# Performance work log

Measured on AMD Instinct MI355X. Metric: run time of the kernel, lower is better.

The kernel has to match this reference:

```python
import jax, jax.numpy as jnp
import numpy as np

N_USERS = 100_000
N_ITEMS = 50_000
N_NODES = N_USERS + N_ITEMS
D = 64
NUM_LAYERS = 3
N_INTER = 1_000_000  # interactions; symmetrized -> 2M directed edges
BATCH = 4096


def setup_inputs() -> dict:
    key = jax.random.key(0)
    k_u, k_i, k_r, k_c, k_uid, k_iid = jax.random.split(key, 6)
    user_embedding = jax.random.normal(k_u, (N_USERS, D), dtype=jnp.float32)
    item_embedding = jax.random.normal(k_i, (N_ITEMS, D), dtype=jnp.float32)

    # build symmetric normalized adjacency edges as in get_norm_adj_mat
    rng = np.random.default_rng(0)
    row = rng.integers(0, N_USERS, size=N_INTER)
    col = rng.integers(0, N_ITEMS, size=N_INTER) + N_USERS
    src = np.concatenate([row, col])
    dst = np.concatenate([col, row])
    deg = np.bincount(src, minlength=N_NODES).astype(np.float32)
    norm_deg = 1.0 / np.sqrt(np.where(deg == 0, 1.0, deg))
    edge_weight = (norm_deg[src] * norm_deg[dst]).astype(np.float32)
    edge_index = np.stack([src, dst]).astype(np.int64)

    user_id = jax.random.randint(k_uid, (BATCH,), 0, N_USERS)
    item_id = jax.random.randint(k_iid, (BATCH,), 0, N_ITEMS)
    return {
        "user_embedding": user_embedding,
        "item_embedding": item_embedding,
        "edge_weight": jnp.asarray(edge_weight),
        "edge_index": jnp.asarray(edge_index),
        "user_id": user_id,
        "item_id": item_id,
    }


def reference(user_embedding, item_embedding, edge_weight, edge_index, user_id, item_id):
    # ego embeddings: [N_NODES, D]
    x = jnp.concatenate([user_embedding, item_embedding], axis=0)
    src, dst = edge_index[0], edge_index[1]
    h = x
    acc = x  # running sum over layer outputs (incl. layer 0)
    for _ in range(NUM_LAYERS):
        # LightGCNConv: gather source, scale by edge weight, scatter-add to dest
        msg = h[src] * edge_weight[:, None]                       # [E, D]
        h = jax.ops.segment_sum(msg, dst, num_segments=N_NODES)   # [N, D]
        acc = acc + h
    final = acc / jnp.asarray(NUM_LAYERS + 1, dtype=x.dtype)      # mean over layers
    u_embed = final[:N_USERS][user_id]
    i_embed = final[N_USERS:][item_id]
    return (u_embed, i_embed)
```

## Files before the change

kernel.cpp:

```cpp
#include <hip/hip_runtime.h>

#define N_USERS 100000
#define N_NODES 150000
#define DIM 64
#define BATCH 4096
#define BSHIFT 8
#define BUCKET 256
#define NB 586
#define NBP 768
#define PAIRS_PER_BLK 2048
#define STRIP 4096
#define CAPSHIFT 13
#define CAP (1 << CAPSHIFT)

typedef unsigned short bf16_t;

static __device__ __forceinline__ float bf2f(bf16_t h) {
    return __uint_as_float(((unsigned)h) << 16);
}
static __device__ __forceinline__ bf16_t f2bf(float f) {
    unsigned u = __float_as_uint(f);
    return (bf16_t)((u + 0x7FFFu + ((u >> 16) & 1u)) >> 16);
}

__global__ void __launch_bounds__(256)
lgcn_bin(const int* __restrict__ row, const int* __restrict__ col,
         int* __restrict__ pos, int* __restrict__ binned, int EH) {
    __shared__ int cnt[NBP];
    __shared__ int sA[256], sB[256];
    __shared__ int base[NB + 2];
    __shared__ int stage[STRIP];
    int tid = threadIdx.x;
    int k = blockIdx.x;
    cnt[tid] = 0; cnt[tid + 256] = 0; cnt[tid + 512] = 0;
    __syncthreads();
    int e0 = k * PAIRS_PER_BLK;
    int e1 = min(EH, e0 + PAIRS_PER_BLK);
    int n = e1 - e0;
    int nq = n >> 2;
    const int4* r4 = (const int4*)(row + e0);
    const int4* c4 = (const int4*)(col + e0);
    for (int q = tid; q < nq; q += 256) {
        int4 r = r4[q]; int4 c = c4[q];
        atomicAdd(&cnt[r.x >> BSHIFT], 1); atomicAdd(&cnt[c.x >> BSHIFT], 1);
        atomicAdd(&cnt[r.y >> BSHIFT], 1); atomicAdd(&cnt[c.y >> BSHIFT], 1);
        atomicAdd(&cnt[r.z >> BSHIFT], 1); atomicAdd(&cnt[c.z >> BSHIFT], 1);
        atomicAdd(&cnt[r.w >> BSHIFT], 1); atomicAdd(&cnt[c.w >> BSHIFT], 1);
    }
    __syncthreads();
    int c0 = cnt[3 * tid], c1 = cnt[3 * tid + 1], c2 = cnt[3 * tid + 2];
    int s = c0 + c1 + c2;
    sA[tid] = s;
    __syncthreads();
    int* c_ = sA; int* n_ = sB;
    for (int off = 1; off < 256; off <<= 1) {
        n_[tid] = (tid >= off) ? c_[tid] + c_[tid - off] : c_[tid];
        __syncthreads();
        int* t = c_; c_ = n_; n_ = t;
    }
    int excl = c_[tid] - s;
    if (3 * tid     <= NB) base[3 * tid]     = excl;
    if (3 * tid + 1 <= NB) base[3 * tid + 1] = excl + c0;
    if (3 * tid + 2 <= NB) base[3 * tid + 2] = excl + c0 + c1;
    __syncthreads();
    for (int i = tid; i <= NB; i += 256) {
        pos[k * (NB + 1) + i] = base[i];
        cnt[i] = base[i];
    }
    __syncthreads();
    for (int q = tid; q < nq; q += 256) {
        int4 r = r4[q]; int4 c = c4[q];
        int rr[4] = { r.x, r.y, r.z, r.w };
        int cc[4] = { c.x, c.y, c.z, c.w };
#pragma unroll
        for (int j = 0; j < 4; ++j) {
            int p1 = atomicAdd(&cnt[cc[j] >> BSHIFT], 1);
            stage[p1] = ((cc[j] & (BUCKET - 1)) << 18) | rr[j];
            int p2 = atomicAdd(&cnt[rr[j] >> BSHIFT], 1);
            stage[p2] = ((rr[j] & (BUCKET - 1)) << 18) | cc[j];
        }
    }
    __syncthreads();
    int m4 = (2 * n) >> 2;
    int4* dst = (int4*)(binned + k * STRIP);
    const int4* st4 = (const int4*)stage;
    for (int j = tid; j < m4; j += 256) dst[j] = st4[j];
}

__global__ void __launch_bounds__(256)
lgcn_build_csr(const int* __restrict__ pos, const int* __restrict__ binned,
               int4* __restrict__ nodeinfo, int* __restrict__ packed,
               const float* __restrict__ ue, const float* __restrict__ ie,
               bf16_t* __restrict__ g0, bf16_t* __restrict__ g1, int nblk) {
    __shared__ int stage[CAP];
    __shared__ int sorted[CAP];
    __shared__ int sA[256], sB[256];
    __shared__ int hist[256], cur[256];
    int b = blockIdx.x;
    int tid = threadIdx.x;
    int a0 = 0, l0 = 0, a1 = 0, l1 = 0;
    if (tid < nblk) {
        const int* pk = pos + tid * (NB + 1) + b;
        a0 = pk[0]; l0 = pk[1] - a0;
    }
    if (tid + 256 < nblk) {
        const int* pk = pos + (tid + 256) * (NB + 1) + b;
        a1 = pk[0]; l1 = pk[1] - a1;
    }
    int u = l0 + l1;
    sA[tid] = u;
    __syncthreads();
    int* c_ = sA; int* n_ = sB;
    for (int off = 1; off < 256; off <<= 1) {
        n_[tid] = (tid >= off) ? c_[tid] + c_[tid - off] : c_[tid];
        __syncthreads();
        int* t = c_; c_ = n_; n_ = t;
    }
    int myBase = c_[tid] - u;
    int Eb = c_[255];
    __syncthreads();
    {
        const int* s0 = binned + tid * STRIP + a0;
        int i = 0;
        for (; i + 4 <= l0; i += 4) {
            int w0 = s0[i], w1 = s0[i + 1], w2 = s0[i + 2], w3 = s0[i + 3];
            stage[myBase + i] = w0;     stage[myBase + i + 1] = w1;
            stage[myBase + i + 2] = w2; stage[myBase + i + 3] = w3;
        }
        for (; i < l0; ++i) stage[myBase + i] = s0[i];
        const int* s1 = binned + (tid + 256) * STRIP + a1;
        int bb = myBase + l0;
        i = 0;
        for (; i + 4 <= l1; i += 4) {
            int w0 = s1[i], w1 = s1[i + 1], w2 = s1[i + 2], w3 = s1[i + 3];
            stage[bb + i] = w0;     stage[bb + i + 1] = w1;
            stage[bb + i + 2] = w2; stage[bb + i + 3] = w3;
        }
        for (; i < l1; ++i) stage[bb + i] = s1[i];
    }
    hist[tid] = 0;
    __syncthreads();
    for (int j = tid; j < Eb; j += 256)
        atomicAdd(&hist[stage[j] >> 18], 1);
    __syncthreads();
    int deg = hist[tid];
    int degp = (deg + 3) & ~3;
    sA[tid] = degp;
    __syncthreads();
    int* c2 = sA; int* n2 = sB;
    for (int off = 1; off < 256; off <<= 1) {
        n2[tid] = (tid >= off) ? c2[tid] + c2[tid - off] : c2[tid];
        __syncthreads();
        int* t = c2; c2 = n2; n2 = t;
    }
    int startLoc = c2[tid] - degp;
    int totPad = c2[255];
    cur[tid] = startLoc;
    int gstart = (b << CAPSHIFT) + startLoc;
    int node = (b << BSHIFT) + tid;
    float da = (deg == 0) ? 1.0f : (float)deg;
    float sq = sqrtf(da);
    float nm = 1.0f / sq;
    if (node < N_NODES) {
        int4 ni;
        ni.x = gstart;
        ni.y = deg;
        ni.z = __float_as_int(nm);
        ni.w = __float_as_int(sq);
        nodeinfo[node] = ni;
    }
    __syncthreads();
    hist[tid] = __float_as_int(nm);
    for (int j = tid; j < totPad; j += 256) sorted[j] = N_NODES;
    __syncthreads();
    for (int j = tid; j < Eb; j += 256) {
        int w = stage[j];
        int p = atomicAdd(&cur[w >> 18], 1);
        sorted[p] = w & 0x3FFFF;
    }
    __syncthreads();
    int4* dst = (int4*)(packed + (b << CAPSHIFT));
    const int4* s4 = (const int4*)sorted;
    for (int j = tid; j < (totPad >> 2); j += 256) dst[j] = s4[j];
    int firstNode = b << BSHIFT;
    int nloc = min(BUCKET, N_NODES - firstNode);
    const int nU16 = N_USERS * (DIM / 4);
    int t0 = firstNode * (DIM / 4);
    for (int i = tid; i < nloc * (DIM / 4); i += 256) {
        int t = t0 + i;
        float4 x = (t < nU16) ? ((const float4*)ue)[t]
                              : ((const float4*)ie)[t - nU16];
        float nrm = __int_as_float(hist[i >> 4]);
        ushort4 o;
        o.x = f2bf(x.x * nrm); o.y = f2bf(x.y * nrm);
        o.z = f2bf(x.z * nrm); o.w = f2bf(x.w * nrm);
        ((ushort4*)g0)[t] = o;
    }
    if (b == 0 && tid < 32) {
        const int nT = N_NODES * (DIM / 4);
        if (tid < 16) ((ushort4*)g0)[nT + tid] = make_ushort4(0, 0, 0, 0);
        else          ((ushort4*)g1)[nT + tid - 16] = make_ushort4(0, 0, 0, 0);
    }
}


static __device__ __forceinline__ float4
gather_sum(const bf16_t* __restrict__ g, const int* __restrict__ packed,
           int start, int deg, int grp, int c) {
    float4 acc = make_float4(0.f, 0.f, 0.f, 0.f);
    for (int o = 4 * grp; o < deg; o += 16) {
        int4 e4 = *(const int4*)(packed + start + o);
        ushort4 v0 = ((const ushort4*)(g + (size_t)e4.x * DIM))[c];
        ushort4 v1 = ((const ushort4*)(g + (size_t)e4.y * DIM))[c];
        ushort4 v2 = ((const ushort4*)(g + (size_t)e4.z * DIM))[c];
        ushort4 v3 = ((const ushort4*)(g + (size_t)e4.w * DIM))[c];
        acc.x += bf2f(v0.x); acc.y += bf2f(v0.y);
        acc.z += bf2f(v0.z); acc.w += bf2f(v0.w);
        acc.x += bf2f(v1.x); acc.y += bf2f(v1.y);
        acc.z += bf2f(v1.z); acc.w += bf2f(v1.w);
        acc.x += bf2f(v2.x); acc.y += bf2f(v2.y);
        acc.z += bf2f(v2.z); acc.w += bf2f(v2.w);
        acc.x += bf2f(v3.x); acc.y += bf2f(v3.y);
        acc.z += bf2f(v3.z); acc.w += bf2f(v3.w);
    }
    return acc;
}

__global__ void __launch_bounds__(256)
lgcn_pull(const bf16_t* __restrict__ g, const int4* __restrict__ nodeinfo,
          const int* __restrict__ packed, bf16_t* __restrict__ gn) {
    int n = blockIdx.x * 4 + (threadIdx.x >> 6);
    if (n >= N_NODES) return;
    int lane = threadIdx.x & 63;
    int grp = lane >> 4;
    int c = lane & 15;
    int4 ni = nodeinfo[n];
    float4 acc = gather_sum(g, packed, ni.x, ni.y, grp, c);
#pragma unroll
    for (int off = 16; off < 64; off <<= 1) {
        acc.x += __shfl_xor(acc.x, off, 64);
        acc.y += __shfl_xor(acc.y, off, 64);
        acc.z += __shfl_xor(acc.z, off, 64);
        acc.w += __shfl_xor(acc.w, off, 64);
    }
    if (lane < 16) {
        float nm = __int_as_float(ni.z);
        float s2 = nm * nm;
        ushort4 o;
        o.x = f2bf(acc.x * s2); o.y = f2bf(acc.y * s2);
        o.z = f2bf(acc.z * s2); o.w = f2bf(acc.w * s2);
        ((ushort4*)(gn + (size_t)n * DIM))[c] = o;
    }
}

__global__ void __launch_bounds__(256)
lgcn_final(const float* __restrict__ ue, const float* __restrict__ ie,
           const bf16_t* __restrict__ g1, const bf16_t* __restrict__ g2,
           const int4* __restrict__ nodeinfo, const int* __restrict__ packed,
           const int* __restrict__ uid, const int* __restrict__ iid,
           float* __restrict__ out) {
    int slot = blockIdx.x * 4 + (threadIdx.x >> 6);
    if (slot >= 2 * BATCH) return;
    int lane = threadIdx.x & 63;
    int grp = lane >> 4;
    int c = lane & 15;
    int isItem = slot >= BATCH;
    int b = isItem ? (slot - BATCH) : slot;
    int node = isItem ? (N_USERS + iid[b]) : uid[b];
    int4 ni = nodeinfo[node];
    float4 acc = gather_sum(g2, packed, ni.x, ni.y, grp, c);
#pragma unroll
    for (int off = 16; off < 64; off <<= 1) {
        acc.x += __shfl_xor(acc.x, off, 64);
        acc.y += __shfl_xor(acc.y, off, 64);
        acc.z += __shfl_xor(acc.z, off, 64);
        acc.w += __shfl_xor(acc.w, off, 64);
    }
    if (lane < 16) {
        const float* xb = isItem ? (ie + (size_t)(node - N_USERS) * DIM)
                                 : (ue + (size_t)node * DIM);
        float4 x = ((const float4*)xb)[c];
        ushort4 a1 = ((const ushort4*)(g1 + (size_t)node * DIM))[c];
        ushort4 a2 = ((const ushort4*)(g2 + (size_t)node * DIM))[c];
        float rn = __int_as_float(ni.w);
        float nm = __int_as_float(ni.z);
        float4 r;
        r.x = 0.25f * (x.x + rn * (bf2f(a1.x) + bf2f(a2.x)) + nm * acc.x);
        r.y = 0.25f * (x.y + rn * (bf2f(a1.y) + bf2f(a2.y)) + nm * acc.y);
        r.z = 0.25f * (x.z + rn * (bf2f(a1.z) + bf2f(a2.z)) + nm * acc.z);
        r.w = 0.25f * (x.w + rn * (bf2f(a1.w) + bf2f(a2.w)) + nm * acc.w);
        ((float4*)(out + (size_t)slot * DIM))[c] = r;
    }
}


extern "C" void kernel_launch(void* const* d_in, const int* in_sizes, int n_in,
                              void* d_out, int out_size, void* d_ws, size_t ws_size,
                              hipStream_t stream) {
    const float* ue  = (const float*)d_in[0];
    const float* ie  = (const float*)d_in[1];
    const int*   ei  = (const int*)d_in[3];
    const int*   uid = (const int*)d_in[4];
    const int*   iid = (const int*)d_in[5];
    float* out = (float*)d_out;

    const int E  = in_sizes[2];
    const int EH = E / 2;
    const int* row = ei;
    const int* col = ei + E;

    const int nblk = (EH + PAIRS_PER_BLK - 1) / PAIRS_PER_BLK;

    char* p = (char*)d_ws;
    size_t off = 0;
    auto carve = [&](size_t bytes) -> char* {
        char* r = p + off;
        off += (bytes + 255) & ~(size_t)255;
        return r;
    };
    const size_t nodeBf16 = (size_t)(N_NODES + 1) * DIM * sizeof(bf16_t);
    bf16_t* gA       = (bf16_t*)carve(nodeBf16);
    bf16_t* gB       = (bf16_t*)carve(nodeBf16);
    int4*   nodeinfo = (int4*)carve((size_t)N_NODES * sizeof(int4));
    int*    pos      = (int*)carve((size_t)nblk * (NB + 1) * sizeof(int));
    int*    binned   = (int*)carve((size_t)nblk * STRIP * sizeof(int));
    int*    packed   = (int*)carve((size_t)NB * CAP * sizeof(int));
    (void)ws_size;

    lgcn_bin<<<nblk, 256, 0, stream>>>(row, col, pos, binned, EH);
    lgcn_build_csr<<<NB, 256, 0, stream>>>(pos, binned, nodeinfo, packed,
                                           ue, ie, gA, gB, nblk);
    const int pullGrid = (N_NODES + 3) / 4;
    lgcn_pull<<<pullGrid, 256, 0, stream>>>(gA, nodeinfo, packed, gB);
    lgcn_pull<<<pullGrid, 256, 0, stream>>>(gB, nodeinfo, packed, gA);
    lgcn_final<<<(2 * BATCH + 3) / 4, 256, 0, stream>>>(
        ue, ie, gB, gA, nodeinfo, packed, uid, iid, out);
}
```

Before: 229.8 us.

## Map one feature per lane in pull gather, drop cross-lane reduction

The neighbor gather changes from four 16-lane groups, each handling a quarter of the edges with 8-byte loads followed by a shuffle reduction, to all 64 lanes reading the same edge row one bf16 element per lane. The edge loop is unrolled by eight with scalar (readfirstlane) indices so the addresses stay uniform. This removes the shuffle reductions and the idle lanes in the epilogue, but each load is now 2 bytes per lane instead of 8 and each wave processes edges sequentially, so the number of memory instructions per edge goes up. Padded degree handling assumes the packed lists are padded to multiples of four with zero-row sentinels.

```diff
diff --git a/kernel.cpp b/kernel.cpp
--- a/kernel.cpp
+++ b/kernel.cpp
@@ -204,24 +204,38 @@
 }
 
 
-static __device__ __forceinline__ float4
-gather_sum(const bf16_t* __restrict__ g, const int* __restrict__ packed,
-           int start, int deg, int grp, int c) {
-    float4 acc = make_float4(0.f, 0.f, 0.f, 0.f);
-    for (int o = 4 * grp; o < deg; o += 16) {
-        int4 e4 = *(const int4*)(packed + start + o);
-        ushort4 v0 = ((const ushort4*)(g + (size_t)e4.x * DIM))[c];
-        ushort4 v1 = ((const ushort4*)(g + (size_t)e4.y * DIM))[c];
-        ushort4 v2 = ((const ushort4*)(g + (size_t)e4.z * DIM))[c];
-        ushort4 v3 = ((const ushort4*)(g + (size_t)e4.w * DIM))[c];
-        acc.x += bf2f(v0.x); acc.y += bf2f(v0.y);
-        acc.z += bf2f(v0.z); acc.w += bf2f(v0.w);
-        acc.x += bf2f(v1.x); acc.y += bf2f(v1.y);
-        acc.z += bf2f(v1.z); acc.w += bf2f(v1.w);
-        acc.x += bf2f(v2.x); acc.y += bf2f(v2.y);
-        acc.z += bf2f(v2.z); acc.w += bf2f(v2.w);
-        acc.x += bf2f(v3.x); acc.y += bf2f(v3.y);
-        acc.z += bf2f(v3.z); acc.w += bf2f(v3.w);
+static __device__ __forceinline__ float
+gather_lane(const bf16_t* __restrict__ g, const int* __restrict__ packed,
+            int su, int dp, int lane) {
+    float acc = 0.f;
+    const int4* p4 = (const int4*)(packed + su);
+    int k = 0;
+    for (; k + 8 <= dp; k += 8) {
+        int4 ea = p4[k >> 2];
+        int4 eb = p4[(k >> 2) + 1];
+        const bf16_t* r0 = g + ((unsigned)ea.x << 6);
+        const bf16_t* r1 = g + ((unsigned)ea.y << 6);
+        const bf16_t* r2 = g + ((unsigned)ea.z << 6);
+        const bf16_t* r3 = g + ((unsigned)ea.w << 6);
+        const bf16_t* r4 = g + ((unsigned)eb.x << 6);
+        const bf16_t* r5 = g + ((unsigned)eb.y << 6);
+        const bf16_t* r6 = g + ((unsigned)eb.z << 6);
+        const bf16_t* r7 = g + ((unsigned)eb.w << 6);
+        float v0 = bf2f(r0[lane]); float v1 = bf2f(r1[lane]);
+        float v2 = bf2f(r2[lane]); float v3 = bf2f(r3[lane]);
+        float v4 = bf2f(r4[lane]); float v5 = bf2f(r5[lane]);
+        float v6 = bf2f(r6[lane]); float v7 = bf2f(r7[lane]);
+        acc += ((v0 + v1) + (v2 + v3)) + ((v4 + v5) + (v6 + v7));
+    }
+    if (k < dp) {
+        int4 ea = p4[k >> 2];
+        const bf16_t* r0 = g + ((unsigned)ea.x << 6);
+        const bf16_t* r1 = g + ((unsigned)ea.y << 6);
+        const bf16_t* r2 = g + ((unsigned)ea.z << 6);
+        const bf16_t* r3 = g + ((unsigned)ea.w << 6);
+        float v0 = bf2f(r0[lane]); float v1 = bf2f(r1[lane]);
+        float v2 = bf2f(r2[lane]); float v3 = bf2f(r3[lane]);
+        acc += (v0 + v1) + (v2 + v3);
     }
     return acc;
 }
@@ -231,26 +245,15 @@
           const int* __restrict__ packed, bf16_t* __restrict__ gn) {
     int n = blockIdx.x * 4 + (threadIdx.x >> 6);
     if (n >= N_NODES) return;
+    n = __builtin_amdgcn_readfirstlane(n);
     int lane = threadIdx.x & 63;
-    int grp = lane >> 4;
-    int c = lane & 15;
     int4 ni = nodeinfo[n];
-    float4 acc = gather_sum(g, packed, ni.x, ni.y, grp, c);
-#pragma unroll
-    for (int off = 16; off < 64; off <<= 1) {
-        acc.x += __shfl_xor(acc.x, off, 64);
-        acc.y += __shfl_xor(acc.y, off, 64);
-        acc.z += __shfl_xor(acc.z, off, 64);
-        acc.w += __shfl_xor(acc.w, off, 64);
-    }
-    if (lane < 16) {
-        float nm = __int_as_float(ni.z);
-        float s2 = nm * nm;
-        ushort4 o;
-        o.x = f2bf(acc.x * s2); o.y = f2bf(acc.y * s2);
-        o.z = f2bf(acc.z * s2); o.w = f2bf(acc.w * s2);
-        ((ushort4*)(gn + (size_t)n * DIM))[c] = o;
-    }
+    int su = __builtin_amdgcn_readfirstlane(ni.x);
+    int du = __builtin_amdgcn_readfirstlane(ni.y);
+    int dp = (du + 3) & ~3;
+    float acc = gather_lane(g, packed, su, dp, lane);
+    float nm = __int_as_float(ni.z);
+    gn[((unsigned)n << 6) + lane] = f2bf(acc * nm * nm);
 }
 
 __global__ void __launch_bounds__(256)
@@ -261,36 +264,25 @@
            float* __restrict__ out) {
     int slot = blockIdx.x * 4 + (threadIdx.x >> 6);
     if (slot >= 2 * BATCH) return;
+    slot = __builtin_amdgcn_readfirstlane(slot);
     int lane = threadIdx.x & 63;
-    int grp = lane >> 4;
-    int c = lane & 15;
     int isItem = slot >= BATCH;
     int b = isItem ? (slot - BATCH) : slot;
     int node = isItem ? (N_USERS + iid[b]) : uid[b];
+    node = __builtin_amdgcn_readfirstlane(node);
     int4 ni = nodeinfo[node];
-    float4 acc = gather_sum(g2, packed, ni.x, ni.y, grp, c);
-#pragma unroll
-    for (int off = 16; off < 64; off <<= 1) {
-        acc.x += __shfl_xor(acc.x, off, 64);
-        acc.y += __shfl_xor(acc.y, off, 64);
-        acc.z += __shfl_xor(acc.z, off, 64);
-        acc.w += __shfl_xor(acc.w, off, 64);
-    }
-    if (lane < 16) {
-        const float* xb = isItem ? (ie + (size_t)(node - N_USERS) * DIM)
-                                 : (ue + (size_t)node * DIM);
-        float4 x = ((const float4*)xb)[c];
-        ushort4 a1 = ((const ushort4*)(g1 + (size_t)node * DIM))[c];
-        ushort4 a2 = ((const ushort4*)(g2 + (size_t)node * DIM))[c];
-        float rn = __int_as_float(ni.w);
-        float nm = __int_as_float(ni.z);
-        float4 r;
-        r.x = 0.25f * (x.x + rn * (bf2f(a1.x) + bf2f(a2.x)) + nm * acc.x);
-        r.y = 0.25f * (x.y + rn * (bf2f(a1.y) + bf2f(a2.y)) + nm * acc.y);
-        r.z = 0.25f * (x.z + rn * (bf2f(a1.z) + bf2f(a2.z)) + nm * acc.z);
-        r.w = 0.25f * (x.w + rn * (bf2f(a1.w) + bf2f(a2.w)) + nm * acc.w);
-        ((float4*)(out + (size_t)slot * DIM))[c] = r;
-    }
+    int su = __builtin_amdgcn_readfirstlane(ni.x);
+    int du = __builtin_amdgcn_readfirstlane(ni.y);
+    int dp = (du + 3) & ~3;
+    float acc = gather_lane(g2, packed, su, dp, lane);
+    const float* xb = isItem ? (ie + ((unsigned)(node - N_USERS) << 6))
+                             : (ue + ((unsigned)node << 6));
+    float x = xb[lane];
+    float a1 = bf2f(g1[((unsigned)node << 6) + lane]);
+    float a2 = bf2f(g2[((unsigned)node << 6) + lane]);
+    float rn = __int_as_float(ni.w);
+    float nm = __int_as_float(ni.z);
+    out[((unsigned)slot << 6) + lane] = 0.25f * (x + rn * (a1 + a2) + nm * acc);
 }
 
 
```

Result: faster. 223.2 us (-2.9%).
